# Kernel optimization log

Measured on AMD Instinct MI355X. Metric: run time of the kernel, lower is better.

The kernel has to match this reference:

```python
import jax, jax.numpy as jnp
import numpy as np

B, L, D, H = 2, 4096, 512, 8
HD = D // H  # head_dim = 64


def setup_inputs() -> dict:
    key = jax.random.key(0)
    ks = jax.random.split(key, 5)
    s = 0.02
    return {
        "x": jax.random.normal(ks[0], (B, L, D), dtype=jnp.float32),
        "w_qkv": jax.random.normal(ks[1], (D, 3 * D), dtype=jnp.float32) * s,
        "b_qkv": jax.random.normal(ks[2], (3 * D,), dtype=jnp.float32) * s,
        "w_o": jax.random.normal(ks[3], (D, D), dtype=jnp.float32) * s,
        "b_o": jax.random.normal(ks[4], (D,), dtype=jnp.float32) * s,
    }


def reference(x, w_qkv, b_qkv, w_o, b_o):
    b, l, _ = x.shape
    # QKV projection, then split heads: [B, L, 3D] -> [B, H, L, 3*HD]
    qkv = x @ w_qkv + b_qkv
    qkv = qkv.reshape(b, l, H, 3 * HD).transpose(0, 2, 1, 3)
    q, k, v = jnp.split(qkv, 3, axis=-1)  # each [B, H, L, HD]
    scale = 1.0 / jnp.sqrt(jnp.asarray(HD, dtype=q.dtype))
    # full score matrix [B, H, L, L], softmax in float32 (matches .float() cast)
    scores = jnp.einsum('bhld,bhsd->bhls', q, k) * scale
    attn = jax.nn.softmax(scores.astype(jnp.float32), axis=-1).astype(q.dtype)
    values = jnp.einsum('bhls,bhsd->bhld', attn, v)  # [B, H, L, HD]
    values = values.transpose(0, 2, 1, 3).reshape(b, l, D)
    return values @ w_o + b_o
```

## Files before the change

### kernel.cpp

```cpp
#include <hip/hip_runtime.h>


#define B_  2
#define L_  4096
#define D_  512
#define H_  8
#define HD_ 64
#define BH_ (B_*H_)
#define M_  (B_*L_)
#define QKVN (3*D_)
#define HEADSZ (BH_*L_*HD_)

typedef unsigned short ushort;
typedef unsigned int uint;
typedef __bf16 bf16x8 __attribute__((ext_vector_type(8)));
typedef float  f32x4  __attribute__((ext_vector_type(4)));

typedef const __attribute__((address_space(1))) void g_void;
typedef __attribute__((address_space(3))) void l_void;

__device__ __forceinline__ ushort f2bf(float f) {
    __bf16 h = (__bf16)f;
    return __builtin_bit_cast(ushort, h);
}

__global__ __launch_bounds__(256)
void prep_k(const float* __restrict__ x, ushort* __restrict__ xb,
            const float* __restrict__ wq, ushort* __restrict__ wtq,
            const float* __restrict__ wo, ushort* __restrict__ wto)
{
    int bid = blockIdx.x, tid = threadIdx.x;
    if (bid < 4096) {
        int idx = bid * 256 + tid;
        float4 v = ((const float4*)x)[idx];
        ushort4 o; o.x = f2bf(v.x); o.y = f2bf(v.y); o.z = f2bf(v.z); o.w = f2bf(v.w);
        ((ushort4*)xb)[idx] = o;
    } else if (bid < 7168) {
        int idx = (bid - 4096) * 256 + tid;
        int c = idx / D_, r = idx % D_;
        wtq[idx] = f2bf(wq[r * QKVN + c]);
    } else {
        int idx = (bid - 7168) * 256 + tid;
        int c = idx / D_, r = idx % D_;
        wto[idx] = f2bf(wo[r * D_ + c]);
    }
}

#define TP 66
__global__ __launch_bounds__(256)
void transpose_v(const ushort* __restrict__ V, ushort* __restrict__ VT) {
    __shared__ ushort T[64 * TP];
    const int tid = threadIdx.x;
    const int bh = blockIdx.y;
    const int l0 = blockIdx.x * 64;
    const int base = bh * (L_ * HD_);
    #pragma unroll
    for (int i = 0; i < 2; i++) {
        int c = i * 256 + tid;
        int l = c >> 3, dc = (c & 7) * 8;
        uint4 v = *(const uint4*)&V[base + (l0 + l) * HD_ + dc];
        uint* p = (uint*)&T[l * TP + dc];
        p[0] = v.x; p[1] = v.y; p[2] = v.z; p[3] = v.w;
    }
    __syncthreads();
    #pragma unroll
    for (int p = 0; p < 2; p++) {
        int c = p * 256 + tid;
        int d = c >> 3, lb = c & 7;
        ushort tmp[8];
        #pragma unroll
        for (int j = 0; j < 8; j++) tmp[j] = T[(lb * 8 + j) * TP + d];
        *(uint4*)&VT[base + d * L_ + l0 + lb * 8] = *(uint4*)tmp;
    }
}

__global__ __launch_bounds__(256)
void gemm_bt(const ushort* __restrict__ A, const ushort* __restrict__ Bt,
             const float* __restrict__ bias, void* __restrict__ out,
             int M, int N, int K, int mode)
{
    __shared__ ushort As[128 * 32];
    __shared__ ushort Bs[128 * 32];

    const int tid  = threadIdx.x;
    const int lane = tid & 63;
    const int wid  = tid >> 6;
    const int wm   = wid >> 1, wn = wid & 1;
    const int lr   = lane & 15;
    const int quad = lane >> 4;
    const int tm = blockIdx.x, tn = blockIdx.y;

    f32x4 acc[4][4] = {};
    const int arow = tm * 128;
    const int brow = tn * 128;

    for (int k0 = 0; k0 < K; k0 += 32) {
        #pragma unroll
        for (int i = 0; i < 2; i++) {
            int c   = i * 256 + tid;
            int row = c >> 2;
            int kk  = (c & 3) * 8;
            __builtin_amdgcn_global_load_lds(
                (g_void*)&A[(size_t)(arow + row) * K + k0 + kk],
                (l_void*)&As[c * 8], 16, 0, 0);
            __builtin_amdgcn_global_load_lds(
                (g_void*)&Bt[(size_t)(brow + row) * K + k0 + kk],
                (l_void*)&Bs[c * 8], 16, 0, 0);
        }
        __syncthreads();

        bf16x8 af[4], bfr[4];
        #pragma unroll
        for (int t = 0; t < 4; t++) {
            af [t] = *(const bf16x8*)&As[(wm * 64 + t * 16 + lr) * 32 + quad * 8];
            bfr[t] = *(const bf16x8*)&Bs[(wn * 64 + t * 16 + lr) * 32 + quad * 8];
        }
        #pragma unroll
        for (int mt = 0; mt < 4; mt++)
            #pragma unroll
            for (int nt = 0; nt < 4; nt++)
                acc[mt][nt] = __builtin_amdgcn_mfma_f32_16x16x32_bf16(
                    af[mt], bfr[nt], acc[mt][nt], 0, 0, 0);
        __syncthreads();
    }

    #pragma unroll
    for (int nt = 0; nt < 4; nt++) {
        int col = tn * 128 + wn * 64 + nt * 16 + lr;
        float bv = bias[col];
        #pragma unroll
        for (int mt = 0; mt < 4; mt++) {
            #pragma unroll
            for (int r = 0; r < 4; r++) {
                int row = tm * 128 + wm * 64 + mt * 16 + quad * 4 + r;
                float v = acc[mt][nt][r] + bv;
                if (mode == 0) {
                    ((float*)out)[(size_t)row * N + col] = v;
                } else {
                    int d = col & 63;
                    int g = col >> 6;
                    int which = g % 3;
                    int h = g / 3;
                    int b = row >> 12;
                    int l = row & (L_ - 1);
                    ((ushort*)out)[which * HEADSZ + (((b * H_ + h) * L_ + l) * HD_) + d]
                        = f2bf(v);
                }
            }
        }
    }
}

#define SP 72
__global__ __launch_bounds__(512)
void attn_k(const ushort* __restrict__ Q, const ushort* __restrict__ K,
            const ushort* __restrict__ VT, ushort* __restrict__ O)
{
    __shared__ ushort Ks[2][64 * SP];
    __shared__ ushort Vt[2][64 * SP];
    __shared__ ushort Pw[8][16 * SP];

    const int tid  = threadIdx.x;
    const int lane = tid & 63;
    const int wid  = tid >> 6;
    const int lr   = lane & 15;
    const int quad = lane >> 4;
    const int bh = blockIdx.y;
    const int q0 = blockIdx.x * 128;
    const int base = bh * (L_ * HD_);

    const int rrS = tid >> 3;
    const int ccS = (tid & 7) * 8;

    const int qrow = q0 + wid * 16 + lr;
    const bf16x8 qf0 = *(const bf16x8*)&Q[base + qrow * HD_ +      quad * 8];
    const bf16x8 qf1 = *(const bf16x8*)&Q[base + qrow * HD_ + 32 + quad * 8];

    float l_part[4] = {0.f, 0.f, 0.f, 0.f};
    f32x4 o_acc[4] = {};
    const float C2 = 0.18033688011112042f;

    {
        uint4 a = *(const uint4*)&K [base + rrS * HD_ + ccS];
        uint4 b = *(const uint4*)&VT[base + rrS * L_  + ccS];
        *(uint4*)&Ks[0][rrS * SP + ccS] = a;
        *(uint4*)&Vt[0][rrS * SP + ccS] = b;
    }

    for (int t = 0; t < L_ / 64; t++) {
        const int cur = t & 1;
        __syncthreads();

        uint4 na, nb;
        const bool pf = (t + 1) < (L_ / 64);
        if (pf) {
            int s1 = (t + 1) * 64;
            na = *(const uint4*)&K [base + (s1 + rrS) * HD_ + ccS];
            nb = *(const uint4*)&VT[base + rrS * L_ + s1 + ccS];
        }

        f32x4 sc[4] = {};
        #pragma unroll
        for (int nt = 0; nt < 4; nt++) {
            bf16x8 b0 = *(const bf16x8*)&Ks[cur][(nt * 16 + lr) * SP +      quad * 8];
            bf16x8 b1 = *(const bf16x8*)&Ks[cur][(nt * 16 + lr) * SP + 32 + quad * 8];
            sc[nt] = __builtin_amdgcn_mfma_f32_16x16x32_bf16(qf0, b0, sc[nt], 0, 0, 0);
            sc[nt] = __builtin_amdgcn_mfma_f32_16x16x32_bf16(qf1, b1, sc[nt], 0, 0, 0);
        }

        #pragma unroll
        for (int nt = 0; nt < 4; nt++) {
            #pragma unroll
            for (int r = 0; r < 4; r++) {
                float p = exp2f(sc[nt][r] * C2);
                l_part[r] += p;
                Pw[wid][(quad * 4 + r) * SP + nt * 16 + lr] = f2bf(p);
            }
        }

        #pragma unroll
        for (int ks = 0; ks < 2; ks++) {
            bf16x8 pa = *(const bf16x8*)&Pw[wid][lr * SP + ks * 32 + quad * 8];
            #pragma unroll
            for (int nt = 0; nt < 4; nt++) {
                bf16x8 vb = *(const bf16x8*)&Vt[cur][(nt * 16 + lr) * SP + ks * 32 + quad * 8];
                o_acc[nt] = __builtin_amdgcn_mfma_f32_16x16x32_bf16(pa, vb, o_acc[nt], 0, 0, 0);
            }
        }

        if (pf) {
            *(uint4*)&Ks[cur ^ 1][rrS * SP + ccS] = na;
            *(uint4*)&Vt[cur ^ 1][rrS * SP + ccS] = nb;
        }
    }

    #pragma unroll
    for (int off = 8; off >= 1; off >>= 1)
        #pragma unroll
        for (int r = 0; r < 4; r++)
            l_part[r] += __shfl_xor(l_part[r], off, 64);

    float inv[4];
    #pragma unroll
    for (int r = 0; r < 4; r++) inv[r] = 1.0f / l_part[r];

    const int b = bh >> 3, h = bh & 7;
    #pragma unroll
    for (int nt = 0; nt < 4; nt++) {
        #pragma unroll
        for (int r = 0; r < 4; r++) {
            int row = q0 + wid * 16 + quad * 4 + r;
            int d   = nt * 16 + lr;
            O[((b * L_ + row) * D_) + h * HD_ + d] = f2bf(o_acc[nt][r] * inv[r]);
        }
    }
}

extern "C" void kernel_launch(void* const* d_in, const int* in_sizes, int n_in,
                              void* d_out, int out_size, void* d_ws, size_t ws_size,
                              hipStream_t stream)
{
    const float* x     = (const float*)d_in[0];
    const float* w_qkv = (const float*)d_in[1];
    const float* b_qkv = (const float*)d_in[2];
    const float* w_o   = (const float*)d_in[3];
    const float* b_o   = (const float*)d_in[4];

    char* ws = (char*)d_ws;
    size_t o = 0;
    ushort* xb   = (ushort*)(ws + o); o += (size_t)M_ * D_ * 2;
    ushort* qkv  = (ushort*)(ws + o); o += (size_t)3 * HEADSZ * 2;
    ushort* attn = (ushort*)(ws + o); o += (size_t)M_ * D_ * 2;
    ushort* wtq  = (ushort*)(ws + o); o += (size_t)QKVN * D_ * 2;
    ushort* wto  = (ushort*)(ws + o);
    ushort* vt   = xb;

    hipLaunchKernelGGL(prep_k, dim3(8192), dim3(256), 0, stream,
                       x, xb, w_qkv, wtq, w_o, wto);
    hipLaunchKernelGGL(gemm_bt, dim3(M_ / 128, QKVN / 128), dim3(256), 0, stream,
                       xb, wtq, b_qkv, (void*)qkv, M_, QKVN, D_, 1);
    hipLaunchKernelGGL(transpose_v, dim3(L_ / 64, BH_), dim3(256), 0, stream,
                       qkv + 2 * HEADSZ, vt);
    hipLaunchKernelGGL(attn_k, dim3(L_ / 128, BH_), dim3(512), 0, stream,
                       qkv, qkv + HEADSZ, vt, attn);
    hipLaunchKernelGGL(gemm_bt, dim3(M_ / 128, D_ / 128), dim3(256), 0, stream,
                       attn, wto, b_o, d_out, M_, D_, D_, 0);
}
```

Baseline: 255.3 us.

## Rework attention kernel: 4 waves with 32 query rows each, V loaded directly to registers

The attention kernel now runs 256 threads per block, and each wave handles two 16-row query tiles, so every K fragment read from LDS is reused across two MFMAs. V^T fragments are loaded straight from global memory into registers instead of being staged through LDS. The operands are swapped (K/V as A, Q/P as B) so each lane's scores are contiguous and P can be written with vector stores. The output is staged through LDS for coalesced 16-byte global writes. The trade-offs are higher register pressure, fewer waves per block, and V reads that bypass LDS double-buffering and may expose global latency.

```diff
diff --git a/kernel.cpp b/kernel.cpp
--- a/kernel.cpp
+++ b/kernel.cpp
@@ -152,107 +152,147 @@
 }
 
 #define SP 72
-__global__ __launch_bounds__(512)
+#define PP 72
+__global__ __launch_bounds__(256)
 void attn_k(const ushort* __restrict__ Q, const ushort* __restrict__ K,
             const ushort* __restrict__ VT, ushort* __restrict__ O)
 {
     __shared__ ushort Ks[2][64 * SP];
-    __shared__ ushort Vt[2][64 * SP];
-    __shared__ ushort Pw[8][16 * SP];
+    __shared__ ushort Pw[4][32 * PP];
 
     const int tid  = threadIdx.x;
     const int lane = tid & 63;
     const int wid  = tid >> 6;
     const int lr   = lane & 15;
     const int quad = lane >> 4;
-    const int bh = blockIdx.y;
-    const int q0 = blockIdx.x * 128;
+    const int bh   = blockIdx.y;
+    const int q0   = blockIdx.x * 128;
     const int base = bh * (L_ * HD_);
 
-    const int rrS = tid >> 3;
-    const int ccS = (tid & 7) * 8;
-
-    const int qrow = q0 + wid * 16 + lr;
-    const bf16x8 qf0 = *(const bf16x8*)&Q[base + qrow * HD_ +      quad * 8];
-    const bf16x8 qf1 = *(const bf16x8*)&Q[base + qrow * HD_ + 32 + quad * 8];
-
-    float l_part[4] = {0.f, 0.f, 0.f, 0.f};
-    f32x4 o_acc[4] = {};
+    bf16x8 qf[2][2];
+    #pragma unroll
+    for (int mt = 0; mt < 2; mt++) {
+        int qrow = q0 + wid * 32 + mt * 16 + lr;
+        qf[mt][0] = *(const bf16x8*)&Q[base + qrow * HD_ +      quad * 8];
+        qf[mt][1] = *(const bf16x8*)&Q[base + qrow * HD_ + 32 + quad * 8];
+    }
+
+    float l_part[2] = {0.f, 0.f};
+    f32x4 o_acc[2][4] = {};
     const float C2 = 0.18033688011112042f;
 
-    {
-        uint4 a = *(const uint4*)&K [base + rrS * HD_ + ccS];
-        uint4 b = *(const uint4*)&VT[base + rrS * L_  + ccS];
-        *(uint4*)&Ks[0][rrS * SP + ccS] = a;
-        *(uint4*)&Vt[0][rrS * SP + ccS] = b;
+    #pragma unroll
+    for (int i = 0; i < 2; i++) {
+        int c = i * 256 + tid;
+        int rr = c >> 3, cc = (c & 7) * 8;
+        *(uint4*)&Ks[0][rr * SP + cc] = *(const uint4*)&K[base + rr * HD_ + cc];
     }
 
     for (int t = 0; t < L_ / 64; t++) {
         const int cur = t & 1;
+        const int s0 = t * 64;
         __syncthreads();
 
-        uint4 na, nb;
+        uint4 na[2];
         const bool pf = (t + 1) < (L_ / 64);
         if (pf) {
-            int s1 = (t + 1) * 64;
-            na = *(const uint4*)&K [base + (s1 + rrS) * HD_ + ccS];
-            nb = *(const uint4*)&VT[base + rrS * L_ + s1 + ccS];
-        }
-
-        f32x4 sc[4] = {};
+            #pragma unroll
+            for (int i = 0; i < 2; i++) {
+                int c = i * 256 + tid;
+                int rr = c >> 3, cc = (c & 7) * 8;
+                na[i] = *(const uint4*)&K[base + (s0 + 64 + rr) * HD_ + cc];
+            }
+        }
+
+        bf16x8 vf[2][4];
+        #pragma unroll
+        for (int ks = 0; ks < 2; ks++)
+            #pragma unroll
+            for (int nt = 0; nt < 4; nt++)
+                vf[ks][nt] = *(const bf16x8*)&VT[base + (nt * 16 + lr) * L_
+                                                 + s0 + ks * 32 + quad * 8];
+
+        f32x4 sc[2][4] = {};
+        #pragma unroll
+        for (int kk = 0; kk < 2; kk++) {
+            #pragma unroll
+            for (int nt = 0; nt < 4; nt++) {
+                bf16x8 kf = *(const bf16x8*)&Ks[cur][(nt * 16 + lr) * SP
+                                                     + kk * 32 + quad * 8];
+                #pragma unroll
+                for (int mt = 0; mt < 2; mt++)
+                    sc[mt][nt] = __builtin_amdgcn_mfma_f32_16x16x32_bf16(
+                        kf, qf[mt][kk], sc[mt][nt], 0, 0, 0);
+            }
+        }
+
+        #pragma unroll
+        for (int mt = 0; mt < 2; mt++) {
+            #pragma unroll
+            for (int nt = 0; nt < 4; nt++) {
+                ushort4 p4;
+                float p0 = exp2f(sc[mt][nt][0] * C2);
+                float p1 = exp2f(sc[mt][nt][1] * C2);
+                float p2 = exp2f(sc[mt][nt][2] * C2);
+                float p3 = exp2f(sc[mt][nt][3] * C2);
+                l_part[mt] += (p0 + p1) + (p2 + p3);
+                p4.x = f2bf(p0); p4.y = f2bf(p1); p4.z = f2bf(p2); p4.w = f2bf(p3);
+                *(ushort4*)&Pw[wid][(mt * 16 + lr) * PP + nt * 16 + quad * 4] = p4;
+            }
+        }
+
+        #pragma unroll
+        for (int mt = 0; mt < 2; mt++) {
+            #pragma unroll
+            for (int ks = 0; ks < 2; ks++) {
+                bf16x8 pfr = *(const bf16x8*)&Pw[wid][(mt * 16 + lr) * PP
+                                                      + ks * 32 + quad * 8];
+                #pragma unroll
+                for (int nt = 0; nt < 4; nt++)
+                    o_acc[mt][nt] = __builtin_amdgcn_mfma_f32_16x16x32_bf16(
+                        vf[ks][nt], pfr, o_acc[mt][nt], 0, 0, 0);
+            }
+        }
+
+        if (pf) {
+            #pragma unroll
+            for (int i = 0; i < 2; i++) {
+                int c = i * 256 + tid;
+                int rr = c >> 3, cc = (c & 7) * 8;
+                *(uint4*)&Ks[cur ^ 1][rr * SP + cc] = na[i];
+            }
+        }
+    }
+
+    #pragma unroll
+    for (int mt = 0; mt < 2; mt++) {
+        l_part[mt] += __shfl_xor(l_part[mt], 16, 64);
+        l_part[mt] += __shfl_xor(l_part[mt], 32, 64);
+    }
+    float inv[2] = {1.0f / l_part[0], 1.0f / l_part[1]};
+
+    #pragma unroll
+    for (int mt = 0; mt < 2; mt++) {
         #pragma unroll
         for (int nt = 0; nt < 4; nt++) {
-            bf16x8 b0 = *(const bf16x8*)&Ks[cur][(nt * 16 + lr) * SP +      quad * 8];
-            bf16x8 b1 = *(const bf16x8*)&Ks[cur][(nt * 16 + lr) * SP + 32 + quad * 8];
-            sc[nt] = __builtin_amdgcn_mfma_f32_16x16x32_bf16(qf0, b0, sc[nt], 0, 0, 0);
-            sc[nt] = __builtin_amdgcn_mfma_f32_16x16x32_bf16(qf1, b1, sc[nt], 0, 0, 0);
-        }
-
-        #pragma unroll
-        for (int nt = 0; nt < 4; nt++) {
-            #pragma unroll
-            for (int r = 0; r < 4; r++) {
-                float p = exp2f(sc[nt][r] * C2);
-                l_part[r] += p;
-                Pw[wid][(quad * 4 + r) * SP + nt * 16 + lr] = f2bf(p);
-            }
-        }
-
-        #pragma unroll
-        for (int ks = 0; ks < 2; ks++) {
-            bf16x8 pa = *(const bf16x8*)&Pw[wid][lr * SP + ks * 32 + quad * 8];
-            #pragma unroll
-            for (int nt = 0; nt < 4; nt++) {
-                bf16x8 vb = *(const bf16x8*)&Vt[cur][(nt * 16 + lr) * SP + ks * 32 + quad * 8];
-                o_acc[nt] = __builtin_amdgcn_mfma_f32_16x16x32_bf16(pa, vb, o_acc[nt], 0, 0, 0);
-            }
-        }
-
-        if (pf) {
-            *(uint4*)&Ks[cur ^ 1][rrS * SP + ccS] = na;
-            *(uint4*)&Vt[cur ^ 1][rrS * SP + ccS] = nb;
-        }
-    }
-
-    #pragma unroll
-    for (int off = 8; off >= 1; off >>= 1)
-        #pragma unroll
-        for (int r = 0; r < 4; r++)
-            l_part[r] += __shfl_xor(l_part[r], off, 64);
-
-    float inv[4];
-    #pragma unroll
-    for (int r = 0; r < 4; r++) inv[r] = 1.0f / l_part[r];
-
+            ushort4 p4;
+            p4.x = f2bf(o_acc[mt][nt][0] * inv[mt]);
+            p4.y = f2bf(o_acc[mt][nt][1] * inv[mt]);
+            p4.z = f2bf(o_acc[mt][nt][2] * inv[mt]);
+            p4.w = f2bf(o_acc[mt][nt][3] * inv[mt]);
+            *(ushort4*)&Pw[wid][(mt * 16 + lr) * PP + nt * 16 + quad * 4] = p4;
+        }
+    }
     const int b = bh >> 3, h = bh & 7;
     #pragma unroll
-    for (int nt = 0; nt < 4; nt++) {
-        #pragma unroll
-        for (int r = 0; r < 4; r++) {
-            int row = q0 + wid * 16 + quad * 4 + r;
-            int d   = nt * 16 + lr;
-            O[((b * L_ + row) * D_) + h * HD_ + d] = f2bf(o_acc[nt][r] * inv[r]);
-        }
+    for (int i = 0; i < 4; i++) {
+        int c = i * 64 + lane;
+        int row = c >> 3, dc = (c & 7) * 8;
+        ushort tmp[8];
+        #pragma unroll
+        for (int j = 0; j < 8; j++) tmp[j] = Pw[wid][row * PP + dc + j];
+        *(uint4*)&O[((size_t)(b * L_ + q0 + wid * 32 + row)) * D_ + h * HD_ + dc]
+            = *(uint4*)tmp;
     }
 }
 
@@ -281,7 +321,7 @@
                        xb, wtq, b_qkv, (void*)qkv, M_, QKVN, D_, 1);
     hipLaunchKernelGGL(transpose_v, dim3(L_ / 64, BH_), dim3(256), 0, stream,
                        qkv + 2 * HEADSZ, vt);
-    hipLaunchKernelGGL(attn_k, dim3(L_ / 128, BH_), dim3(512), 0, stream,
+    hipLaunchKernelGGL(attn_k, dim3(L_ / 128, BH_), dim3(256), 0, stream,
                        qkv, qkv + HEADSZ, vt, attn);
     hipLaunchKernelGGL(gemm_bt, dim3(M_ / 128, D_ / 128), dim3(256), 0, stream,
                        attn, wto, b_o, d_out, M_, D_, D_, 0);
```

New measurement: 292.8 us. 14.7% more time.
